# Kernel tuning notes

Measured on AMD Instinct MI355X. Metric: run time of the kernel, lower is better.

## Reference

```python
import jax, jax.numpy as jnp
import numpy as np

N = 50000          # nodes
E = 500000         # edges
NT = 10000         # target nodes
ET = 100000        # target edges
NS = 128           # node scalar dim (128x0e)
NV = 64            # node vector mult (64x1e); node dim = 128 + 64*3 = 320
ES = 64            # edge scalar dim (64x0e)
EV = 32            # edge vector mult (32x1e); edge dim = 64 + 32*3 = 160
H = 128            # hidden_dim
NA = 32            # num_atom_types
NB = 8             # num_bond_types


def setup_inputs() -> dict:
    key = jax.random.key(0)
    ks = jax.random.split(key, 40)
    nrm = lambda k, s: jax.random.normal(k, s, jnp.float32)
    w = lambda k, fi, fo: nrm(k, (fi, fo)) / np.float32(np.sqrt(fi))
    d = {}
    d['h_final'] = nrm(ks[0], (N, NS + 3 * NV))
    d['e_final'] = nrm(ks[1], (E, ES + 3 * EV))
    d['r_t_final'] = nrm(ks[2], (N, 3))
    d['target_node_idx'] = jax.random.randint(ks[3], (NT,), 0, N)
    d['target_edge_idx'] = jax.random.randint(ks[4], (ET,), 0, E)
    d['edge_index'] = jax.random.randint(ks[5], (2, E), 0, N)
    # node scalar projection (LinearRS on 0e channels)
    d['W_nsp'] = w(ks[6], NS, NS); d['b_nsp'] = jnp.zeros((NS,), jnp.float32)
    # atom type head
    d['W_at1'] = w(ks[7], NS, H); d['b_at1'] = jnp.zeros((H,), jnp.float32)
    d['W_at2'] = w(ks[8], H, NA); d['b_at2'] = jnp.zeros((NA,), jnp.float32)
    # left/right edge linears
    d['W_left'] = w(ks[9], NS, H); d['b_left'] = jnp.zeros((H,), jnp.float32)
    d['W_right'] = w(ks[10], NS, H); d['b_right'] = jnp.zeros((H,), jnp.float32)
    # edge_lin: Linear(ES+EV+H -> H), LayerNorm, SiLU, Linear(H -> 1)
    din = ES + EV + H
    d['W_el1'] = w(ks[11], din, H); d['b_el1'] = jnp.zeros((H,), jnp.float32)
    d['ln_g'] = jnp.ones((H,), jnp.float32); d['ln_b'] = jnp.zeros((H,), jnp.float32)
    d['W_el2'] = w(ks[12], H, 1); d['b_el2'] = jnp.zeros((1,), jnp.float32)
    # fully-connected tensor product to 0e: paths 0e*0e->0e and 1e*1e->0e
    d['w_tp0'] = nrm(ks[13], (NS, NS))
    d['w_tp1'] = nrm(ks[14], (NV, NV))
    # bond head MLP: Linear(1+edge_dim -> H), SiLU, Linear(H -> NB)
    d['W_bh1'] = w(ks[15], 1 + ES + 3 * EV, H); d['b_bh1'] = jnp.zeros((H,), jnp.float32)
    d['W_bh2'] = w(ks[16], H, NB); d['b_bh2'] = jnp.zeros((NB,), jnp.float32)
    return d


def reference(h_final, e_final, r_t_final, target_node_idx, target_edge_idx, edge_index,
              W_nsp, b_nsp, W_at1, b_at1, W_at2, b_at2, W_left, b_left, W_right, b_right,
              W_el1, b_el1, ln_g, ln_b, W_el2, b_el2, w_tp0, w_tp1, W_bh1, b_bh1, W_bh2, b_bh2):
    silu = jax.nn.silu
    node_proj = lambda x: x[:, :NS] @ W_nsp + b_nsp  # LinearRS restricted to 0e channels

    # --- atom type head (target nodes only) ---
    s_t = node_proj(h_final[target_node_idx])
    atom_type_logits = silu(s_t @ W_at1 + b_at1) @ W_at2 + b_at2  # [NT, NA]

    # --- per-edge force prediction ---
    row, col = edge_index[0], edge_index[1]
    hs = node_proj(h_final)                                   # [N, NS]
    inter = (hs[row] @ W_left + b_left) * (hs[col] @ W_right + b_right)  # [E, H]
    e_scalar = e_final[:, :ES]                                # [E, ES]
    e_high = e_final[:, ES:].reshape(-1, EV, 3)               # [E, EV, 3]
    e_high_norms = jnp.sqrt(jnp.sum(e_high * e_high, axis=-1))  # [E, EV]
    x = jnp.concatenate([e_scalar, e_high_norms, inter], axis=-1) @ W_el1 + b_el1
    mu = jnp.mean(x, axis=-1, keepdims=True)
    var = jnp.var(x, axis=-1, keepdims=True)
    x = (x - mu) / jnp.sqrt(var + 1e-5) * ln_g + ln_b         # LayerNorm
    weight_edge = silu(x) @ W_el2 + b_el2                     # [E, 1]
    rel = r_t_final[row] - r_t_final[col]                     # [E, 3]
    dist = jnp.linalg.norm(rel, axis=-1, keepdims=True) + 1e-8
    force = weight_edge * (rel / dist) / (dist + 1.0)
    delta = jax.ops.segment_sum(force, row, num_segments=h_final.shape[0])
    predicted_r0 = (r_t_final + delta)[target_node_idx]       # [NT, 3]

    # --- bond head: fully-connected TP(node, node) -> 0e, then MLP ---
    r2 = edge_index[0][target_edge_idx]
    c2 = edge_index[1][target_edge_idx]
    sx, vx = h_final[r2, :NS], h_final[r2, NS:].reshape(-1, NV, 3)
    sy, vy = h_final[c2, :NS], h_final[c2, NS:].reshape(-1, NV, 3)
    tp = (jnp.einsum('ei,ij,ej->e', sx, w_tp0, sy) / np.float32(NS)
          + jnp.einsum('eid,ij,ejd->e', vx, w_tp1, vy) / np.float32(NV * np.sqrt(3.0)))[:, None]
    bi = jnp.concatenate([tp, e_final[target_edge_idx]], axis=-1)  # [ET, 1+edge_dim]
    bond_logits = silu(bi @ W_bh1 + b_bh1) @ W_bh2 + b_bh2    # [ET, NB]

    return atom_type_logits, predicted_r0, bond_logits
```

## Files before the change

kernel.cpp:

```cpp
#include <hip/hip_runtime.h>
#include <math.h>

#define NN   50000
#define NE   500000
#define NTT  10000
#define ETT  100000
#define HF   320
#define EFW  160
#define NT3  7813
#define GRID3 1024

typedef __attribute__((ext_vector_type(8))) short short8_t;
typedef __attribute__((ext_vector_type(4))) float f32x4;

__device__ __forceinline__ float silu_f(float x) { return x / (1.f + __expf(-x)); }

__device__ __forceinline__ short f2bf(float f) {
    unsigned u = __float_as_uint(f);
    unsigned r = (u + 0x7fffu + ((u >> 16) & 1u)) >> 16;
    return (short)r;
}
__device__ __forceinline__ float bf2f(short s) {
    return __uint_as_float(((unsigned)(unsigned short)s) << 16);
}
__device__ __forceinline__ int swz256(int row, int col) {
    return row * 256 + (((col << 1) ^ ((row & 7) << 4)) >> 1);
}
__device__ __forceinline__ int swz128(int row, int col) {
    return row * 128 + (((col << 1) ^ ((row & 7) << 4)) >> 1);
}

__global__ __launch_bounds__(256) void k0_all(
    const float* __restrict__ W_nsp, const float* __restrict__ b_nsp,
    const float* __restrict__ W_left, const float* __restrict__ b_left,
    const float* __restrict__ W_right, const float* __restrict__ b_right,
    const float* __restrict__ W_at1, const float* __restrict__ b_at1,
    float* __restrict__ Wl, float* __restrict__ bl,
    float* __restrict__ Wr, float* __restrict__ br,
    float* __restrict__ Wc1, float* __restrict__ bc1)
{
    if (blockIdx.x < 64) {
        int idx = blockIdx.x * 256 + threadIdx.x;
        int i = idx >> 7, j = idx & 127;
        float al = 0.f, ar = 0.f;
        for (int k = 0; k < 128; ++k) {
            float w = W_nsp[i * 128 + k];
            al = fmaf(w, W_left[k * 128 + j], al);
            ar = fmaf(w, W_right[k * 128 + j], ar);
        }
        Wl[idx] = al; Wr[idx] = ar;
        if (i == 0) {
            float cl = 0.f, cr = 0.f;
            for (int k = 0; k < 128; ++k) {
                float bn = b_nsp[k];
                cl = fmaf(bn, W_left[k * 128 + j], cl);
                cr = fmaf(bn, W_right[k * 128 + j], cr);
            }
            bl[j] = cl + b_left[j];
            br[j] = cr + b_right[j];
        }
    } else {
        int idx = (blockIdx.x - 64) * 256 + threadIdx.x;
        int i = idx >> 7, j = idx & 127;
        float a = 0.f;
        for (int k = 0; k < 128; ++k)
            a = fmaf(W_nsp[i * 128 + k], W_at1[k * 128 + j], a);
        Wc1[idx] = a;
        if (i == 0) {
            float c = 0.f;
            for (int k = 0; k < 128; ++k)
                c = fmaf(b_nsp[k], W_at1[k * 128 + j], c);
            bc1[j] = c + b_at1[j];
        }
    }
}

#define KP1 136
__global__ __launch_bounds__(256) void k1_mfma(
    const float* __restrict__ h_final,
    const float* __restrict__ Wl, const float* __restrict__ bl,
    const float* __restrict__ Wr, const float* __restrict__ br,
    short* __restrict__ hlb, short* __restrict__ hrb)
{
    __shared__ __align__(16) short sx[64][KP1];
    const int tid = threadIdx.x;
    const int w = tid >> 6, lane = tid & 63, g = lane >> 4, ln = lane & 15;

    short8_t bfr[4][4];
    float bias[4];
    #pragma unroll
    for (int nf = 0; nf < 4; ++nf) {
        int col = w * 64 + nf * 16 + ln;
        const float* Wsrc = (col < 128) ? Wl : Wr;
        int cc = col & 127;
        bias[nf] = (col < 128) ? bl[cc] : br[cc];
        #pragma unroll
        for (int k0 = 0; k0 < 4; ++k0) {
            short8_t bb;
            #pragma unroll
            for (int j = 0; j < 8; ++j)
                bb[j] = f2bf(Wsrc[(k0 * 32 + g * 8 + j) * 128 + cc]);
            bfr[k0][nf] = bb;
        }
    }

    const int base = blockIdx.x * 64;
    {
        const int e = tid >> 2, q = tid & 3;
        const int n = base + e;
        #pragma unroll
        for (int i = 0; i < 8; ++i) {
            float4 v = make_float4(0.f, 0.f, 0.f, 0.f);
            if (n < NN) v = *(const float4*)&h_final[(size_t)n * HF + q * 32 + i * 4];
            short4 s4; s4.x = f2bf(v.x); s4.y = f2bf(v.y); s4.z = f2bf(v.z); s4.w = f2bf(v.w);
            *(short4*)&sx[e][q * 32 + i * 4] = s4;
        }
    }
    __syncthreads();
    f32x4 acc[4][4];
    #pragma unroll
    for (int mf = 0; mf < 4; ++mf)
        #pragma unroll
        for (int nf = 0; nf < 4; ++nf)
            acc[mf][nf] = (f32x4){0.f, 0.f, 0.f, 0.f};
    #pragma unroll
    for (int k0 = 0; k0 < 4; ++k0) {
        short8_t a[4];
        #pragma unroll
        for (int mf = 0; mf < 4; ++mf)
            a[mf] = *(const short8_t*)&sx[mf * 16 + ln][k0 * 32 + g * 8];
        #pragma unroll
        for (int mf = 0; mf < 4; ++mf)
            #pragma unroll
            for (int nf = 0; nf < 4; ++nf)
                acc[mf][nf] = __builtin_amdgcn_mfma_f32_16x16x32_bf16(
                    a[mf], bfr[k0][nf], acc[mf][nf], 0, 0, 0);
    }
    #pragma unroll
    for (int mf = 0; mf < 4; ++mf)
        #pragma unroll
        for (int nf = 0; nf < 4; ++nf) {
            int col = w * 64 + nf * 16 + ln;
            #pragma unroll
            for (int r = 0; r < 4; ++r) {
                int n = base + mf * 16 + g * 4 + r;
                if (n < NN) {
                    short v = f2bf(acc[mf][nf][r] + bias[nf]);
                    if (col < 128) hlb[(size_t)n * 128 + col] = v;
                    else           hrb[(size_t)n * 128 + col - 128] = v;
                }
            }
        }
}

__global__ __launch_bounds__(256) void k2_mfma(
    const float* __restrict__ h_final, const int* __restrict__ tn,
    const float* __restrict__ Wc1, const float* __restrict__ bc1,
    const float* __restrict__ W_at2, const float* __restrict__ b_at2,
    float* __restrict__ out)
{
    __shared__ __align__(16) short sxf[64 * 128];
    __shared__ __align__(16) short syf[64 * 128];
    const int tid = threadIdx.x;
    const int w = tid >> 6, lane = tid & 63, g = lane >> 4, ln = lane & 15;

    short8_t bfr1[4][2];
    float biasc[2];
    #pragma unroll
    for (int nf = 0; nf < 2; ++nf) {
        int col = w * 32 + nf * 16 + ln;
        biasc[nf] = bc1[col];
        #pragma unroll
        for (int k0 = 0; k0 < 4; ++k0) {
            short8_t bb;
            #pragma unroll
            for (int j = 0; j < 8; ++j)
                bb[j] = f2bf(Wc1[(k0 * 32 + g * 8 + j) * 128 + col]);
            bfr1[k0][nf] = bb;
        }
    }
    short8_t bfr2[4][2];
    float ba2v[2];
    #pragma unroll
    for (int nf = 0; nf < 2; ++nf) {
        ba2v[nf] = b_at2[nf * 16 + ln];
        #pragma unroll
        for (int k0 = 0; k0 < 4; ++k0) {
            short8_t bb;
            #pragma unroll
            for (int j = 0; j < 8; ++j)
                bb[j] = f2bf(W_at2[(k0 * 32 + g * 8 + j) * 32 + nf * 16 + ln]);
            bfr2[k0][nf] = bb;
        }
    }

    const int base = blockIdx.x * 64;
    {
        const int e = tid >> 2, q = tid & 3;
        const int t = base + e;
        const bool valid = (t < NTT);
        const int node = valid ? tn[t] : 0;
        #pragma unroll
        for (int i = 0; i < 8; ++i) {
            float4 v = make_float4(0.f, 0.f, 0.f, 0.f);
            if (valid) v = *(const float4*)&h_final[(size_t)node * HF + q * 32 + i * 4];
            short4 s4; s4.x = f2bf(v.x); s4.y = f2bf(v.y); s4.z = f2bf(v.z); s4.w = f2bf(v.w);
            *(short4*)&sxf[swz128(e, q * 32 + i * 4)] = s4;
        }
    }
    __syncthreads();
    f32x4 acc[4][2];
    #pragma unroll
    for (int mf = 0; mf < 4; ++mf)
        #pragma unroll
        for (int nf = 0; nf < 2; ++nf)
            acc[mf][nf] = (f32x4){0.f, 0.f, 0.f, 0.f};
    #pragma unroll
    for (int k0 = 0; k0 < 4; ++k0) {
        short8_t a[4];
        #pragma unroll
        for (int mf = 0; mf < 4; ++mf)
            a[mf] = *(const short8_t*)&sxf[swz128(mf * 16 + ln, k0 * 32 + g * 8)];
        #pragma unroll
        for (int mf = 0; mf < 4; ++mf)
            #pragma unroll
            for (int nf = 0; nf < 2; ++nf)
                acc[mf][nf] = __builtin_amdgcn_mfma_f32_16x16x32_bf16(
                    a[mf], bfr1[k0][nf], acc[mf][nf], 0, 0, 0);
    }
    #pragma unroll
    for (int mf = 0; mf < 4; ++mf)
        #pragma unroll
        for (int nf = 0; nf < 2; ++nf)
            #pragma unroll
            for (int r = 0; r < 4; ++r)
                syf[swz128(mf * 16 + g * 4 + r, w * 32 + nf * 16 + ln)] =
                    f2bf(silu_f(acc[mf][nf][r] + biasc[nf]));
    __syncthreads();
    f32x4 z[2];
    z[0] = (f32x4){0.f,0.f,0.f,0.f}; z[1] = (f32x4){0.f,0.f,0.f,0.f};
    #pragma unroll
    for (int k0 = 0; k0 < 4; ++k0) {
        short8_t a2 = *(const short8_t*)&syf[swz128(w * 16 + ln, k0 * 32 + g * 8)];
        #pragma unroll
        for (int nf = 0; nf < 2; ++nf)
            z[nf] = __builtin_amdgcn_mfma_f32_16x16x32_bf16(a2, bfr2[k0][nf], z[nf], 0, 0, 0);
    }
    #pragma unroll
    for (int nf = 0; nf < 2; ++nf)
        #pragma unroll
        for (int r = 0; r < 4; ++r) {
            int t = base + w * 16 + g * 4 + r;
            if (t < NTT) out[(size_t)t * 32 + nf * 16 + ln] = z[nf][r] + ba2v[nf];
        }
}

__global__ __launch_bounds__(256) void k3pre(
    const float* __restrict__ e_final, short* __restrict__ Xn)
{
    const int tid = threadIdx.x;
    const int e = blockIdx.x * 32 + (tid >> 3);
    const int sub = tid & 7;
    const float* p = &e_final[(size_t)e * EFW + 64 + sub * 12];
    float4 a = *(const float4*)p;
    float4 b = *(const float4*)(p + 4);
    float4 c = *(const float4*)(p + 8);
    short4 o;
    o.x = f2bf(sqrtf(a.x*a.x + a.y*a.y + a.z*a.z));
    o.y = f2bf(sqrtf(a.w*a.w + b.x*b.x + b.y*b.y));
    o.z = f2bf(sqrtf(b.z*b.z + b.w*b.w + c.x*c.x));
    o.w = f2bf(sqrtf(c.y*c.y + c.z*c.z + c.w*c.w));
    *(short4*)&Xn[(size_t)e * 32 + sub * 4] = o;
}

__global__ __launch_bounds__(512, 4) void k3_edge(
    const float* __restrict__ e_final, const int* __restrict__ edge_index,
    const short* __restrict__ Xn,
    const short* __restrict__ hlb, const short* __restrict__ hrb,
    const float* __restrict__ r_t,
    const float* __restrict__ W_el1, const float* __restrict__ b_el1,
    const float* __restrict__ ln_g, const float* __restrict__ ln_b,
    const float* __restrict__ W_el2, const float* __restrict__ b_el2,
    float* __restrict__ delta)
{
    __shared__ __align__(16) char smem[64 * 256 * 2];
    short* sxf = (short*)smem;
    float* syf = (float*)smem;
    __shared__ float slng[128], slnb[128], sw2[128];
    __shared__ float srel[64][4];
    __shared__ int   sidx[64];

    const int tid  = threadIdx.x;
    const int w    = tid >> 6;
    const int lane = tid & 63;
    const int g    = lane >> 4;
    const int ln   = lane & 15;
    const int es   = tid >> 3, qs = tid & 7;

    if (tid < 128) { slng[tid] = ln_g[tid]; slnb[tid] = ln_b[tid]; sw2[tid] = W_el2[tid]; }

    short8_t bfr[7];
    #pragma unroll
    for (int k0 = 0; k0 < 7; ++k0) {
        short8_t bb;
        #pragma unroll
        for (int j = 0; j < 8; ++j)
            bb[j] = f2bf(W_el1[(k0 * 32 + g * 8 + j) * 128 + w * 16 + ln]);
        bfr[k0] = bb;
    }
    const float bias0 = b_el1[w * 16 + ln];
    const float b2 = b_el2[0];

    for (int t = blockIdx.x; t < NT3; t += GRID3) {
        __syncthreads();

        {
            const int ge = t * 64 + es;
            const bool valid = (ge < NE);
            int r = 0, c = 0;
            if (valid) { r = edge_index[ge]; c = edge_index[NE + ge]; }
            #pragma unroll
            for (int i = 0; i < 2; ++i) {
                float4 v = make_float4(0.f, 0.f, 0.f, 0.f);
                if (valid) v = *(const float4*)&e_final[(size_t)ge * EFW + qs * 8 + i * 4];
                short4 s4; s4.x = f2bf(v.x); s4.y = f2bf(v.y);
                s4.z = f2bf(v.z); s4.w = f2bf(v.w);
                *(short4*)&sxf[swz256(es, qs * 8 + i * 4)] = s4;
            }
            {
                short4 n0 = make_short4(0,0,0,0);
                if (valid) n0 = *(const short4*)&Xn[(size_t)ge * 32 + qs * 4];
                *(short4*)&sxf[swz256(es, 64 + qs * 4)] = n0;
            }
            #pragma unroll
            for (int i = 0; i < 2; ++i) {
                short8_t hv, rv, pr;
                if (valid) {
                    hv = *(const short8_t*)&hlb[(size_t)r * 128 + qs * 16 + i * 8];
                    rv = *(const short8_t*)&hrb[(size_t)c * 128 + qs * 16 + i * 8];
                } else {
                    #pragma unroll
                    for (int jj = 0; jj < 8; ++jj) { hv[jj] = 0; rv[jj] = 0; }
                }
                #pragma unroll
                for (int jj = 0; jj < 8; ++jj)
                    pr[jj] = f2bf(bf2f(hv[jj]) * bf2f(rv[jj]));
                *(short8_t*)&sxf[swz256(es, 96 + qs * 16 + i * 8)] = pr;
            }
            if (qs == 0) {
                float rx = 0.f, ry = 0.f, rz = 0.f;
                if (valid) {
                    rx = r_t[r*3+0] - r_t[c*3+0];
                    ry = r_t[r*3+1] - r_t[c*3+1];
                    rz = r_t[r*3+2] - r_t[c*3+2];
                }
                sidx[es] = r;
                srel[es][0] = rx; srel[es][1] = ry; srel[es][2] = rz;
            }
        }
        __syncthreads();

        f32x4 acc[4];
        #pragma unroll
        for (int mf = 0; mf < 4; ++mf)
            acc[mf] = (f32x4){0.f, 0.f, 0.f, 0.f};
        #pragma unroll
        for (int k0 = 0; k0 < 7; ++k0) {
            short8_t a[4];
            #pragma unroll
            for (int mf = 0; mf < 4; ++mf)
                a[mf] = *(const short8_t*)&sxf[swz256(mf * 16 + ln, k0 * 32 + g * 8)];
            #pragma unroll
            for (int mf = 0; mf < 4; ++mf)
                acc[mf] = __builtin_amdgcn_mfma_f32_16x16x32_bf16(
                    a[mf], bfr[k0], acc[mf], 0, 0, 0);
        }
        __syncthreads();

        #pragma unroll
        for (int mf = 0; mf < 4; ++mf)
            #pragma unroll
            for (int r = 0; r < 4; ++r) {
                int row = mf * 16 + g * 4 + r;
                int col = (w * 16 + ln) ^ ((row & 7) << 2);
                syf[row * 128 + col] = acc[mf][r] + bias0;
            }
        __syncthreads();

        {
            float yv[16];
            float s = 0.f, q = 0.f;
            #pragma unroll
            for (int i = 0; i < 4; ++i) {
                int col4 = (qs * 16 + i * 4) ^ ((es & 7) << 2);
                float4 v = *(const float4*)&syf[es * 128 + col4];
                yv[i*4+0] = v.x; yv[i*4+1] = v.y; yv[i*4+2] = v.z; yv[i*4+3] = v.w;
                s += v.x + v.y + v.z + v.w;
                q += v.x*v.x + v.y*v.y + v.z*v.z + v.w*v.w;
            }
            s += __shfl_xor(s, 1); q += __shfl_xor(q, 1);
            s += __shfl_xor(s, 2); q += __shfl_xor(q, 2);
            s += __shfl_xor(s, 4); q += __shfl_xor(q, 4);
            const float mu = s * (1.f / 128.f);
            const float iv = rsqrtf(q * (1.f / 128.f) - mu * mu + 1e-5f);
            float p = 0.f;
            #pragma unroll
            for (int i = 0; i < 4; ++i) {
                int c0 = qs * 16 + i * 4;
                float4 gv = *(const float4*)&slng[c0];
                float4 bv = *(const float4*)&slnb[c0];
                float4 wv = *(const float4*)&sw2[c0];
                p += silu_f((yv[i*4+0] - mu) * iv * gv.x + bv.x) * wv.x;
                p += silu_f((yv[i*4+1] - mu) * iv * gv.y + bv.y) * wv.y;
                p += silu_f((yv[i*4+2] - mu) * iv * gv.z + bv.z) * wv.z;
                p += silu_f((yv[i*4+3] - mu) * iv * gv.w + bv.w) * wv.w;
            }
            p += __shfl_xor(p, 1); p += __shfl_xor(p, 2); p += __shfl_xor(p, 4);
            if (qs == 0) {
                int ge = t * 64 + es;
                if (ge < NE) {
                    float we = p + b2;
                    float rx = srel[es][0], ry = srel[es][1], rz = srel[es][2];
                    float d = sqrtf(rx*rx + ry*ry + rz*rz) + 1e-8f;
                    float f = we / (d * (d + 1.f));
                    int rr = sidx[es];
                    atomicAdd(&delta[rr*3+0], f*rx);
                    atomicAdd(&delta[rr*3+1], f*ry);
                    atomicAdd(&delta[rr*3+2], f*rz);
                }
            }
        }
    }
}

__global__ __launch_bounds__(256) void k4a_g(
    const float* __restrict__ h_final, const float* __restrict__ w_tp0,
    short* __restrict__ Gb)
{
    __shared__ __align__(16) short sx[64][KP1];
    const int tid = threadIdx.x;
    const int w = tid >> 6, lane = tid & 63, g = lane >> 4, ln = lane & 15;

    short8_t bfr[4][2];
    #pragma unroll
    for (int k0 = 0; k0 < 4; ++k0)
        #pragma unroll
        for (int nf = 0; nf < 2; ++nf) {
            short8_t bb;
            #pragma unroll
            for (int j = 0; j < 8; ++j)
                bb[j] = f2bf(w_tp0[(k0 * 32 + g * 8 + j) * 128 + w * 32 + nf * 16 + ln]);
            bfr[k0][nf] = bb;
        }

    const int base = blockIdx.x * 64;
    {
        const int e = tid >> 2, q = tid & 3;
        const int n = base + e;
        #pragma unroll
        for (int i = 0; i < 8; ++i) {
            float4 v = make_float4(0.f, 0.f, 0.f, 0.f);
            if (n < NN) v = *(const float4*)&h_final[(size_t)n * HF + q * 32 + i * 4];
            short4 s4; s4.x = f2bf(v.x); s4.y = f2bf(v.y); s4.z = f2bf(v.z); s4.w = f2bf(v.w);
            *(short4*)&sx[e][q * 32 + i * 4] = s4;
        }
    }
    __syncthreads();
    f32x4 acc[4][2];
    #pragma unroll
    for (int mf = 0; mf < 4; ++mf)
        #pragma unroll
        for (int nf = 0; nf < 2; ++nf)
            acc[mf][nf] = (f32x4){0.f, 0.f, 0.f, 0.f};
    #pragma unroll
    for (int k0 = 0; k0 < 4; ++k0) {
        short8_t a[4];
        #pragma unroll
        for (int mf = 0; mf < 4; ++mf)
            a[mf] = *(const short8_t*)&sx[mf * 16 + ln][k0 * 32 + g * 8];
        #pragma unroll
        for (int mf = 0; mf < 4; ++mf)
            #pragma unroll
            for (int nf = 0; nf < 2; ++nf)
                acc[mf][nf] = __builtin_amdgcn_mfma_f32_16x16x32_bf16(
                    a[mf], bfr[k0][nf], acc[mf][nf], 0, 0, 0);
    }
    #pragma unroll
    for (int mf = 0; mf < 4; ++mf)
        #pragma unroll
        for (int nf = 0; nf < 2; ++nf) {
            int col = w * 32 + nf * 16 + ln;
            #pragma unroll
            for (int r = 0; r < 4; ++r) {
                int n = base + mf * 16 + g * 4 + r;
                if (n < NN) Gb[(size_t)n * 128 + col] = f2bf(acc[mf][nf][r]);
            }
        }
}

__global__ __launch_bounds__(256) void k4b_gv(
    const float* __restrict__ h_final, const float* __restrict__ w_tp1,
    short* __restrict__ Gvb)
{
    __shared__ float sW1T[64 * 65];
    __shared__ float sv[4][192];
    const int tid = threadIdx.x, w = tid >> 6, lane = tid & 63;
    for (int idx = tid; idx < 4096; idx += 256) {
        int i = idx >> 6, j = idx & 63;
        sW1T[j * 65 + i] = w_tp1[idx];
    }
    for (int base = blockIdx.x * 4; base < NN; base += gridDim.x * 4) {
        __syncthreads();
        if (tid < 192) {
            int nd = tid / 48, c4 = tid % 48;
            int n = base + nd;
            float4 v = make_float4(0.f, 0.f, 0.f, 0.f);
            if (n < NN) v = *(const float4*)&h_final[(size_t)n * HF + 128 + c4 * 4];
            *(float4*)&sv[nd][c4 * 4] = v;
        }
        __syncthreads();
        int n = base + w;
        if (n < NN) {
            float a0 = 0.f, a1 = 0.f, a2 = 0.f;
            for (int j = 0; j < 64; ++j) {
                float wv = sW1T[j * 65 + lane];
                a0 = fmaf(wv, sv[w][3 * j],     a0);
                a1 = fmaf(wv, sv[w][3 * j + 1], a1);
                a2 = fmaf(wv, sv[w][3 * j + 2], a2);
            }
            short* gp = &Gvb[(size_t)n * 192 + lane * 3];
            gp[0] = f2bf(a0); gp[1] = f2bf(a1); gp[2] = f2bf(a2);
        }
    }
}

#define KP5 200
__global__ __launch_bounds__(256) void k5_mfma(
    const float* __restrict__ e_final, const int* __restrict__ te,
    const float* __restrict__ h_final, const int* __restrict__ edge_index,
    const short* __restrict__ Gb, const short* __restrict__ Gvb,
    const float* __restrict__ W_bh1, const float* __restrict__ b_bh1,
    const float* __restrict__ W_bh2, const float* __restrict__ b_bh2,
    float* __restrict__ out)
{
    __shared__ __align__(16) short sx[64][KP5];
    __shared__ __align__(16) short sy[64][136];
    __shared__ float stp[64];
    const int tid = threadIdx.x, w = tid >> 6, lane = tid & 63, g = lane >> 4, ln = lane & 15;
    const int base = blockIdx.x * 64;

    {
        const int e = tid >> 2, q = tid & 3;
        const int ge = base + e;
        const bool valid = (ge < ETT);
        const int gid = valid ? te[ge] : 0;
        const int r2 = edge_index[gid], c2 = edge_index[NE + gid];
        float s1 = 0.f, s2 = 0.f;
        #pragma unroll
        for (int i = 0; i < 4; ++i) {
            short8_t gv = *(const short8_t*)&Gb[(size_t)r2 * 128 + q * 32 + i * 8];
            float4 h0 = *(const float4*)&h_final[(size_t)c2 * HF + q * 32 + i * 8];
            float4 h1 = *(const float4*)&h_final[(size_t)c2 * HF + q * 32 + i * 8 + 4];
            s1 += bf2f(gv[0])*h0.x + bf2f(gv[1])*h0.y + bf2f(gv[2])*h0.z + bf2f(gv[3])*h0.w
                + bf2f(gv[4])*h1.x + bf2f(gv[5])*h1.y + bf2f(gv[6])*h1.z + bf2f(gv[7])*h1.w;
        }
        #pragma unroll
        for (int i = 0; i < 6; ++i) {
            short8_t gv = *(const short8_t*)&Gvb[(size_t)c2 * 192 + q * 48 + i * 8];
            float4 h0 = *(const float4*)&h_final[(size_t)r2 * HF + 128 + q * 48 + i * 8];
            float4 h1 = *(const float4*)&h_final[(size_t)r2 * HF + 128 + q * 48 + i * 8 + 4];
            s2 += bf2f(gv[0])*h0.x + bf2f(gv[1])*h0.y + bf2f(gv[2])*h0.z + bf2f(gv[3])*h0.w
                + bf2f(gv[4])*h1.x + bf2f(gv[5])*h1.y + bf2f(gv[6])*h1.z + bf2f(gv[7])*h1.w;
        }
        float res = s1 * (1.f / 128.f) + s2 * (1.f / 110.85125168440814f);
        res += __shfl_xor(res, 1); res += __shfl_xor(res, 2);
        if (q == 0) stp[e] = res;
    }

    short8_t bfr[6][2];
    #pragma unroll
    for (int k0 = 0; k0 < 6; ++k0)
        #pragma unroll
        for (int nf = 0; nf < 2; ++nf) {
            short8_t bb;
            #pragma unroll
            for (int j = 0; j < 8; ++j) {
                int k = k0 * 32 + g * 8 + j;
                float v = 0.f;
                if (k < 160)       v = W_bh1[(size_t)(k + 1) * 128 + w * 32 + nf * 16 + ln];
                else if (k == 160) v = W_bh1[w * 32 + nf * 16 + ln];
                bb[j] = f2bf(v);
            }
            bfr[k0][nf] = bb;
        }
    const float bias0 = b_bh1[w * 32 + ln];
    const float bias1 = b_bh1[w * 32 + 16 + ln];

    short8_t bfr2[4];
    #pragma unroll
    for (int k0 = 0; k0 < 4; ++k0) {
        short8_t bb;
        #pragma unroll
        for (int j = 0; j < 8; ++j) {
            int k = k0 * 32 + g * 8 + j;
            bb[j] = (ln < 8) ? f2bf(W_bh2[k * 8 + ln]) : (short)0;
        }
        bfr2[k0] = bb;
    }
    const float b2o = (ln < 8) ? b_bh2[ln] : 0.f;

    for (int idx = tid; idx < 64 * 39; idx += 256) {
        int rr = idx / 39, c = 161 + idx % 39;
        sx[rr][c] = 0;
    }
    {
        const int e = tid >> 2, q = tid & 3;
        const int ge = base + e;
        const bool valid = (ge < ETT);
        const int gid = valid ? te[ge] : 0;
        #pragma unroll
        for (int i = 0; i < 10; ++i) {
            float4 v = make_float4(0.f, 0.f, 0.f, 0.f);
            if (valid) v = *(const float4*)&e_final[(size_t)gid * EFW + q * 40 + i * 4];
            short4 s4; s4.x = f2bf(v.x); s4.y = f2bf(v.y); s4.z = f2bf(v.z); s4.w = f2bf(v.w);
            *(short4*)&sx[e][q * 40 + i * 4] = s4;
        }
    }
    __syncthreads();
    if (tid < 64) sx[tid][160] = f2bf(stp[tid]);
    __syncthreads();

    f32x4 acc[4][2];
    #pragma unroll
    for (int mf = 0; mf < 4; ++mf)
        #pragma unroll
        for (int nf = 0; nf < 2; ++nf)
            acc[mf][nf] = (f32x4){0.f, 0.f, 0.f, 0.f};
    #pragma unroll
    for (int k0 = 0; k0 < 6; ++k0) {
        short8_t a[4];
        #pragma unroll
        for (int mf = 0; mf < 4; ++mf)
            a[mf] = *(const short8_t*)&sx[mf * 16 + ln][k0 * 32 + g * 8];
        #pragma unroll
        for (int mf = 0; mf < 4; ++mf)
            #pragma unroll
            for (int nf = 0; nf < 2; ++nf)
                acc[mf][nf] = __builtin_amdgcn_mfma_f32_16x16x32_bf16(
                    a[mf], bfr[k0][nf], acc[mf][nf], 0, 0, 0);
    }
    #pragma unroll
    for (int mf = 0; mf < 4; ++mf)
        #pragma unroll
        for (int nf = 0; nf < 2; ++nf)
            #pragma unroll
            for (int r = 0; r < 4; ++r)
                sy[mf * 16 + g * 4 + r][w * 32 + nf * 16 + ln] =
                    f2bf(silu_f(acc[mf][nf][r] + (nf ? bias1 : bias0)));
    __syncthreads();

    f32x4 z = (f32x4){0.f, 0.f, 0.f, 0.f};
    #pragma unroll
    for (int k0 = 0; k0 < 4; ++k0) {
        short8_t a2 = *(const short8_t*)&sy[w * 16 + ln][k0 * 32 + g * 8];
        z = __builtin_amdgcn_mfma_f32_16x16x32_bf16(a2, bfr2[k0], z, 0, 0, 0);
    }
    #pragma unroll
    for (int r = 0; r < 4; ++r) {
        int e = base + w * 16 + g * 4 + r;
        if (ln < 8 && e < ETT) out[(size_t)e * 8 + ln] = z[r] + b2o;
    }
}

__global__ void k6_r0(const float* __restrict__ r_t, const float* __restrict__ delta,
                      const int* __restrict__ tn, float* __restrict__ out)
{
    int i = blockIdx.x * 256 + threadIdx.x;
    if (i < NTT * 3) {
        int t = i / 3, d = i - t * 3;
        int n = tn[t];
        out[i] = r_t[n * 3 + d] + delta[n * 3 + d];
    }
}

extern "C" void kernel_launch(void* const* d_in, const int* in_sizes, int n_in,
                              void* d_out, int out_size, void* d_ws, size_t ws_size,
                              hipStream_t stream)
{
    const float* h_final = (const float*)d_in[0];
    const float* e_final = (const float*)d_in[1];
    const float* r_t     = (const float*)d_in[2];
    const int*   tn      = (const int*)d_in[3];
    const int*   te      = (const int*)d_in[4];
    const int*   ei      = (const int*)d_in[5];
    const float* W_nsp   = (const float*)d_in[6];
    const float* b_nsp   = (const float*)d_in[7];
    const float* W_at1   = (const float*)d_in[8];
    const float* b_at1   = (const float*)d_in[9];
    const float* W_at2   = (const float*)d_in[10];
    const float* b_at2   = (const float*)d_in[11];
    const float* W_left  = (const float*)d_in[12];
    const float* b_left  = (const float*)d_in[13];
    const float* W_right = (const float*)d_in[14];
    const float* b_right = (const float*)d_in[15];
    const float* W_el1   = (const float*)d_in[16];
    const float* b_el1   = (const float*)d_in[17];
    const float* ln_g    = (const float*)d_in[18];
    const float* ln_b    = (const float*)d_in[19];
    const float* W_el2   = (const float*)d_in[20];
    const float* b_el2   = (const float*)d_in[21];
    const float* w_tp0   = (const float*)d_in[22];
    const float* w_tp1   = (const float*)d_in[23];
    const float* W_bh1   = (const float*)d_in[24];
    const float* b_bh1   = (const float*)d_in[25];
    const float* W_bh2   = (const float*)d_in[26];
    const float* b_bh2   = (const float*)d_in[27];

    float* ws    = (float*)d_ws;
    float* Wl    = ws;
    float* bl    = Wl + 16384;
    float* Wr    = bl + 128;
    float* br    = Wr + 16384;
    float* Wc1   = ws + 33024;
    float* bc1   = Wc1 + 16384;
    short* hlb   = (short*)(ws + 49536);
    short* hrb   = hlb + 6400000;
    short* Xn    = hrb + 6400000;
    float* delta = (float*)(Xn + 16000000);
    float* tpb   = delta + 150000;
    short* Gvb   = (short*)(tpb + 100000);
    short* Gb    = hlb;

    float* out      = (float*)d_out;
    float* out_atom = out;
    float* out_r0   = out + 320000;
    float* out_bond = out + 350000;

    k0_all<<<128, 256, 0, stream>>>(W_nsp, b_nsp, W_left, b_left, W_right, b_right,
                                    W_at1, b_at1, Wl, bl, Wr, br, Wc1, bc1);
    k3pre<<<15625, 256, 0, stream>>>(e_final, Xn);
    k1_mfma<<<782, 256, 0, stream>>>(h_final, Wl, bl, Wr, br, hlb, hrb);
    k2_mfma<<<157, 256, 0, stream>>>(h_final, tn, Wc1, bc1, W_at2, b_at2, out_atom);
    hipMemsetAsync(delta, 0, 150000 * sizeof(float), stream);
    k3_edge<<<GRID3, 512, 0, stream>>>(e_final, ei, Xn, hlb, hrb, r_t, W_el1, b_el1,
                                       ln_g, ln_b, W_el2, b_el2, delta);
    k6_r0<<<(NTT * 3 + 255) / 256, 256, 0, stream>>>(r_t, delta, tn, out_r0);
    k4a_g<<<782, 256, 0, stream>>>(h_final, w_tp0, Gb);
    k4b_gv<<<2048, 256, 0, stream>>>(h_final, w_tp1, Gvb);
    k5_mfma<<<1563, 256, 0, stream>>>(e_final, te, h_final, ei, Gb, Gvb,
                                      W_bh1, b_bh1, W_bh2, b_bh2, out_bond);
}
```

Baseline: 416.4 us.

## Merge independent kernels into fewer launches via block-index dispatch

Independent kernels are combined into fused launches that branch on block index. Weight precompute, edge-norm preprocessing and delta zeroing form one launch. The left/right projection, atom head and Gv tensor-product precompute form a second, and the Gb precompute plus the r0 gather form a third. This cuts the launch count from nine (plus a memset) to five and lets independent work from different stages share the GPU. The price is heavier per-launch register and shared-memory footprints, which can lower occupancy for the lighter branches. The Gv precompute also moves ahead of the edge kernel.

```diff
diff --git a/kernel.cpp b/kernel.cpp
--- a/kernel.cpp
+++ b/kernel.cpp
@@ -30,247 +30,279 @@
     return row * 128 + (((col << 1) ^ ((row & 7) << 4)) >> 1);
 }
 
-__global__ __launch_bounds__(256) void k0_all(
+#define KP1 136
+__global__ __launch_bounds__(256) void ka_pre(
+    const float* __restrict__ e_final, short* __restrict__ Xn,
     const float* __restrict__ W_nsp, const float* __restrict__ b_nsp,
     const float* __restrict__ W_left, const float* __restrict__ b_left,
     const float* __restrict__ W_right, const float* __restrict__ b_right,
     const float* __restrict__ W_at1, const float* __restrict__ b_at1,
     float* __restrict__ Wl, float* __restrict__ bl,
     float* __restrict__ Wr, float* __restrict__ br,
-    float* __restrict__ Wc1, float* __restrict__ bc1)
+    float* __restrict__ Wc1, float* __restrict__ bc1,
+    float* __restrict__ delta)
 {
-    if (blockIdx.x < 64) {
-        int idx = blockIdx.x * 256 + threadIdx.x;
-        int i = idx >> 7, j = idx & 127;
-        float al = 0.f, ar = 0.f;
-        for (int k = 0; k < 128; ++k) {
-            float w = W_nsp[i * 128 + k];
-            al = fmaf(w, W_left[k * 128 + j], al);
-            ar = fmaf(w, W_right[k * 128 + j], ar);
-        }
-        Wl[idx] = al; Wr[idx] = ar;
-        if (i == 0) {
-            float cl = 0.f, cr = 0.f;
+    const int tid = threadIdx.x;
+    const int vb = blockIdx.x;
+    if (vb < 15625) {
+        const int e = vb * 32 + (tid >> 3);
+        const int sub = tid & 7;
+        const float* p = &e_final[(size_t)e * EFW + 64 + sub * 12];
+        float4 a = *(const float4*)p;
+        float4 b = *(const float4*)(p + 4);
+        float4 c = *(const float4*)(p + 8);
+        short4 o;
+        o.x = f2bf(sqrtf(a.x*a.x + a.y*a.y + a.z*a.z));
+        o.y = f2bf(sqrtf(a.w*a.w + b.x*b.x + b.y*b.y));
+        o.z = f2bf(sqrtf(b.z*b.z + b.w*b.w + c.x*c.x));
+        o.w = f2bf(sqrtf(c.y*c.y + c.z*c.z + c.w*c.w));
+        *(short4*)&Xn[(size_t)e * 32 + sub * 4] = o;
+    } else if (vb < 15753) {
+        const int b0 = vb - 15625;
+        if (b0 < 64) {
+            int idx = b0 * 256 + tid;
+            int i = idx >> 7, j = idx & 127;
+            float al = 0.f, ar = 0.f;
             for (int k = 0; k < 128; ++k) {
-                float bn = b_nsp[k];
-                cl = fmaf(bn, W_left[k * 128 + j], cl);
-                cr = fmaf(bn, W_right[k * 128 + j], cr);
-            }
-            bl[j] = cl + b_left[j];
-            br[j] = cr + b_right[j];
+                float w = W_nsp[i * 128 + k];
+                al = fmaf(w, W_left[k * 128 + j], al);
+                ar = fmaf(w, W_right[k * 128 + j], ar);
+            }
+            Wl[idx] = al; Wr[idx] = ar;
+            if (i == 0) {
+                float cl = 0.f, cr = 0.f;
+                for (int k = 0; k < 128; ++k) {
+                    float bn = b_nsp[k];
+                    cl = fmaf(bn, W_left[k * 128 + j], cl);
+                    cr = fmaf(bn, W_right[k * 128 + j], cr);
+                }
+                bl[j] = cl + b_left[j];
+                br[j] = cr + b_right[j];
+            }
+        } else {
+            int idx = (b0 - 64) * 256 + tid;
+            int i = idx >> 7, j = idx & 127;
+            float a = 0.f;
+            for (int k = 0; k < 128; ++k)
+                a = fmaf(W_nsp[i * 128 + k], W_at1[k * 128 + j], a);
+            Wc1[idx] = a;
+            if (i == 0) {
+                float c = 0.f;
+                for (int k = 0; k < 128; ++k)
+                    c = fmaf(b_nsp[k], W_at1[k * 128 + j], c);
+                bc1[j] = c + b_at1[j];
+            }
         }
     } else {
-        int idx = (blockIdx.x - 64) * 256 + threadIdx.x;
-        int i = idx >> 7, j = idx & 127;
-        float a = 0.f;
-        for (int k = 0; k < 128; ++k)
-            a = fmaf(W_nsp[i * 128 + k], W_at1[k * 128 + j], a);
-        Wc1[idx] = a;
-        if (i == 0) {
-            float c = 0.f;
-            for (int k = 0; k < 128; ++k)
-                c = fmaf(b_nsp[k], W_at1[k * 128 + j], c);
-            bc1[j] = c + b_at1[j];
-        }
-    }
-}
-
-#define KP1 136
-__global__ __launch_bounds__(256) void k1_mfma(
-    const float* __restrict__ h_final,
+        int i = (vb - 15753) * 256 + tid;
+        if (i < 150000) delta[i] = 0.f;
+    }
+}
+
+__global__ __launch_bounds__(256) void kb_mid(
+    const float* __restrict__ h_final, const int* __restrict__ tn,
     const float* __restrict__ Wl, const float* __restrict__ bl,
     const float* __restrict__ Wr, const float* __restrict__ br,
-    short* __restrict__ hlb, short* __restrict__ hrb)
+    const float* __restrict__ Wc1, const float* __restrict__ bc1,
+    const float* __restrict__ W_at2, const float* __restrict__ b_at2,
+    const float* __restrict__ w_tp1,
+    short* __restrict__ hlb, short* __restrict__ hrb,
+    short* __restrict__ Gvb, float* __restrict__ out_atom)
 {
-    __shared__ __align__(16) short sx[64][KP1];
+    __shared__ __align__(16) char smemB[32768];
     const int tid = threadIdx.x;
-    const int w = tid >> 6, lane = tid & 63, g = lane >> 4, ln = lane & 15;
-
-    short8_t bfr[4][4];
-    float bias[4];
-    #pragma unroll
-    for (int nf = 0; nf < 4; ++nf) {
-        int col = w * 64 + nf * 16 + ln;
-        const float* Wsrc = (col < 128) ? Wl : Wr;
-        int cc = col & 127;
-        bias[nf] = (col < 128) ? bl[cc] : br[cc];
-        #pragma unroll
-        for (int k0 = 0; k0 < 4; ++k0) {
-            short8_t bb;
-            #pragma unroll
-            for (int j = 0; j < 8; ++j)
-                bb[j] = f2bf(Wsrc[(k0 * 32 + g * 8 + j) * 128 + cc]);
-            bfr[k0][nf] = bb;
-        }
-    }
-
-    const int base = blockIdx.x * 64;
-    {
-        const int e = tid >> 2, q = tid & 3;
-        const int n = base + e;
-        #pragma unroll
-        for (int i = 0; i < 8; ++i) {
-            float4 v = make_float4(0.f, 0.f, 0.f, 0.f);
-            if (n < NN) v = *(const float4*)&h_final[(size_t)n * HF + q * 32 + i * 4];
-            short4 s4; s4.x = f2bf(v.x); s4.y = f2bf(v.y); s4.z = f2bf(v.z); s4.w = f2bf(v.w);
-            *(short4*)&sx[e][q * 32 + i * 4] = s4;
-        }
-    }
-    __syncthreads();
-    f32x4 acc[4][4];
-    #pragma unroll
-    for (int mf = 0; mf < 4; ++mf)
-        #pragma unroll
-        for (int nf = 0; nf < 4; ++nf)
-            acc[mf][nf] = (f32x4){0.f, 0.f, 0.f, 0.f};
-    #pragma unroll
-    for (int k0 = 0; k0 < 4; ++k0) {
-        short8_t a[4];
-        #pragma unroll
-        for (int mf = 0; mf < 4; ++mf)
-            a[mf] = *(const short8_t*)&sx[mf * 16 + ln][k0 * 32 + g * 8];
-        #pragma unroll
-        for (int mf = 0; mf < 4; ++mf)
-            #pragma unroll
-            for (int nf = 0; nf < 4; ++nf)
-                acc[mf][nf] = __builtin_amdgcn_mfma_f32_16x16x32_bf16(
-                    a[mf], bfr[k0][nf], acc[mf][nf], 0, 0, 0);
-    }
-    #pragma unroll
-    for (int mf = 0; mf < 4; ++mf)
+    const int vb = blockIdx.x;
+    if (vb < 2048) {
+        float* sW1T = (float*)smemB;
+        float (*sv)[192] = (float(*)[192])(smemB + 16640);
+        const int w = tid >> 6, lane = tid & 63;
+        for (int idx = tid; idx < 4096; idx += 256) {
+            int i = idx >> 6, j = idx & 63;
+            sW1T[j * 65 + i] = w_tp1[idx];
+        }
+        for (int base = vb * 4; base < NN; base += 2048 * 4) {
+            __syncthreads();
+            if (tid < 192) {
+                int nd = tid / 48, c4 = tid % 48;
+                int n = base + nd;
+                float4 v = make_float4(0.f, 0.f, 0.f, 0.f);
+                if (n < NN) v = *(const float4*)&h_final[(size_t)n * HF + 128 + c4 * 4];
+                *(float4*)&sv[nd][c4 * 4] = v;
+            }
+            __syncthreads();
+            int n = base + w;
+            if (n < NN) {
+                float a0 = 0.f, a1 = 0.f, a2 = 0.f;
+                for (int j = 0; j < 64; ++j) {
+                    float wv = sW1T[j * 65 + lane];
+                    a0 = fmaf(wv, sv[w][3 * j],     a0);
+                    a1 = fmaf(wv, sv[w][3 * j + 1], a1);
+                    a2 = fmaf(wv, sv[w][3 * j + 2], a2);
+                }
+                short* gp = &Gvb[(size_t)n * 192 + lane * 3];
+                gp[0] = f2bf(a0); gp[1] = f2bf(a1); gp[2] = f2bf(a2);
+            }
+        }
+    } else if (vb < 2830) {
+        short (*sx)[KP1] = (short(*)[KP1])smemB;
+        const int w = tid >> 6, lane = tid & 63, g = lane >> 4, ln = lane & 15;
+        short8_t bfr[4][4];
+        float bias[4];
         #pragma unroll
         for (int nf = 0; nf < 4; ++nf) {
             int col = w * 64 + nf * 16 + ln;
+            const float* Wsrc = (col < 128) ? Wl : Wr;
+            int cc = col & 127;
+            bias[nf] = (col < 128) ? bl[cc] : br[cc];
+            #pragma unroll
+            for (int k0 = 0; k0 < 4; ++k0) {
+                short8_t bb;
+                #pragma unroll
+                for (int j = 0; j < 8; ++j)
+                    bb[j] = f2bf(Wsrc[(k0 * 32 + g * 8 + j) * 128 + cc]);
+                bfr[k0][nf] = bb;
+            }
+        }
+        const int base = (vb - 2048) * 64;
+        {
+            const int e = tid >> 2, q = tid & 3;
+            const int n = base + e;
+            #pragma unroll
+            for (int i = 0; i < 8; ++i) {
+                float4 v = make_float4(0.f, 0.f, 0.f, 0.f);
+                if (n < NN) v = *(const float4*)&h_final[(size_t)n * HF + q * 32 + i * 4];
+                short4 s4; s4.x = f2bf(v.x); s4.y = f2bf(v.y); s4.z = f2bf(v.z); s4.w = f2bf(v.w);
+                *(short4*)&sx[e][q * 32 + i * 4] = s4;
+            }
+        }
+        __syncthreads();
+        f32x4 acc[4][4];
+        #pragma unroll
+        for (int mf = 0; mf < 4; ++mf)
+            #pragma unroll
+            for (int nf = 0; nf < 4; ++nf)
+                acc[mf][nf] = (f32x4){0.f, 0.f, 0.f, 0.f};
+        #pragma unroll
+        for (int k0 = 0; k0 < 4; ++k0) {
+            short8_t a[4];
+            #pragma unroll
+            for (int mf = 0; mf < 4; ++mf)
+                a[mf] = *(const short8_t*)&sx[mf * 16 + ln][k0 * 32 + g * 8];
+            #pragma unroll
+            for (int mf = 0; mf < 4; ++mf)
+                #pragma unroll
+                for (int nf = 0; nf < 4; ++nf)
+                    acc[mf][nf] = __builtin_amdgcn_mfma_f32_16x16x32_bf16(
+                        a[mf], bfr[k0][nf], acc[mf][nf], 0, 0, 0);
+        }
+        #pragma unroll
+        for (int mf = 0; mf < 4; ++mf)
+            #pragma unroll
+            for (int nf = 0; nf < 4; ++nf) {
+                int col = w * 64 + nf * 16 + ln;
+                #pragma unroll
+                for (int r = 0; r < 4; ++r) {
+                    int n = base + mf * 16 + g * 4 + r;
+                    if (n < NN) {
+                        short v = f2bf(acc[mf][nf][r] + bias[nf]);
+                        if (col < 128) hlb[(size_t)n * 128 + col] = v;
+                        else           hrb[(size_t)n * 128 + col - 128] = v;
+                    }
+                }
+            }
+    } else {
+        short* sxf = (short*)smemB;
+        short* syf = (short*)(smemB + 16384);
+        const int w = tid >> 6, lane = tid & 63, g = lane >> 4, ln = lane & 15;
+        short8_t bfr1[4][2];
+        float biasc[2];
+        #pragma unroll
+        for (int nf = 0; nf < 2; ++nf) {
+            int col = w * 32 + nf * 16 + ln;
+            biasc[nf] = bc1[col];
+            #pragma unroll
+            for (int k0 = 0; k0 < 4; ++k0) {
+                short8_t bb;
+                #pragma unroll
+                for (int j = 0; j < 8; ++j)
+                    bb[j] = f2bf(Wc1[(k0 * 32 + g * 8 + j) * 128 + col]);
+                bfr1[k0][nf] = bb;
+            }
+        }
+        short8_t bfr2[4][2];
+        float ba2v[2];
+        #pragma unroll
+        for (int nf = 0; nf < 2; ++nf) {
+            ba2v[nf] = b_at2[nf * 16 + ln];
+            #pragma unroll
+            for (int k0 = 0; k0 < 4; ++k0) {
+                short8_t bb;
+                #pragma unroll
+                for (int j = 0; j < 8; ++j)
+                    bb[j] = f2bf(W_at2[(k0 * 32 + g * 8 + j) * 32 + nf * 16 + ln]);
+                bfr2[k0][nf] = bb;
+            }
+        }
+        const int base = (vb - 2830) * 64;
+        {
+            const int e = tid >> 2, q = tid & 3;
+            const int t = base + e;
+            const bool valid = (t < NTT);
+            const int node = valid ? tn[t] : 0;
+            #pragma unroll
+            for (int i = 0; i < 8; ++i) {
+                float4 v = make_float4(0.f, 0.f, 0.f, 0.f);
+                if (valid) v = *(const float4*)&h_final[(size_t)node * HF + q * 32 + i * 4];
+                short4 s4; s4.x = f2bf(v.x); s4.y = f2bf(v.y); s4.z = f2bf(v.z); s4.w = f2bf(v.w);
+                *(short4*)&sxf[swz128(e, q * 32 + i * 4)] = s4;
+            }
+        }
+        __syncthreads();
+        f32x4 acc[4][2];
+        #pragma unroll
+        for (int mf = 0; mf < 4; ++mf)
+            #pragma unroll
+            for (int nf = 0; nf < 2; ++nf)
+                acc[mf][nf] = (f32x4){0.f, 0.f, 0.f, 0.f};
+        #pragma unroll
+        for (int k0 = 0; k0 < 4; ++k0) {
+            short8_t a[4];
+            #pragma unroll
+            for (int mf = 0; mf < 4; ++mf)
+                a[mf] = *(const short8_t*)&sxf[swz128(mf * 16 + ln, k0 * 32 + g * 8)];
+            #pragma unroll
+            for (int mf = 0; mf < 4; ++mf)
+                #pragma unroll
+                for (int nf = 0; nf < 2; ++nf)
+                    acc[mf][nf] = __builtin_amdgcn_mfma_f32_16x16x32_bf16(
+                        a[mf], bfr1[k0][nf], acc[mf][nf], 0, 0, 0);
+        }
+        #pragma unroll
+        for (int mf = 0; mf < 4; ++mf)
+            #pragma unroll
+            for (int nf = 0; nf < 2; ++nf)
+                #pragma unroll
+                for (int r = 0; r < 4; ++r)
+                    syf[swz128(mf * 16 + g * 4 + r, w * 32 + nf * 16 + ln)] =
+                        f2bf(silu_f(acc[mf][nf][r] + biasc[nf]));
+        __syncthreads();
+        f32x4 z[2];
+        z[0] = (f32x4){0.f,0.f,0.f,0.f}; z[1] = (f32x4){0.f,0.f,0.f,0.f};
+        #pragma unroll
+        for (int k0 = 0; k0 < 4; ++k0) {
+            short8_t a2 = *(const short8_t*)&syf[swz128(w * 16 + ln, k0 * 32 + g * 8)];
+            #pragma unroll
+            for (int nf = 0; nf < 2; ++nf)
+                z[nf] = __builtin_amdgcn_mfma_f32_16x16x32_bf16(a2, bfr2[k0][nf], z[nf], 0, 0, 0);
+        }
+        #pragma unroll
+        for (int nf = 0; nf < 2; ++nf)
             #pragma unroll
             for (int r = 0; r < 4; ++r) {
-                int n = base + mf * 16 + g * 4 + r;
-                if (n < NN) {
-                    short v = f2bf(acc[mf][nf][r] + bias[nf]);
-                    if (col < 128) hlb[(size_t)n * 128 + col] = v;
-                    else           hrb[(size_t)n * 128 + col - 128] = v;
-                }
-            }
-        }
-}
-
-__global__ __launch_bounds__(256) void k2_mfma(
-    const float* __restrict__ h_final, const int* __restrict__ tn,
-    const float* __restrict__ Wc1, const float* __restrict__ bc1,
-    const float* __restrict__ W_at2, const float* __restrict__ b_at2,
-    float* __restrict__ out)
-{
-    __shared__ __align__(16) short sxf[64 * 128];
-    __shared__ __align__(16) short syf[64 * 128];
-    const int tid = threadIdx.x;
-    const int w = tid >> 6, lane = tid & 63, g = lane >> 4, ln = lane & 15;
-
-    short8_t bfr1[4][2];
-    float biasc[2];
-    #pragma unroll
-    for (int nf = 0; nf < 2; ++nf) {
-        int col = w * 32 + nf * 16 + ln;
-        biasc[nf] = bc1[col];
-        #pragma unroll
-        for (int k0 = 0; k0 < 4; ++k0) {
-            short8_t bb;
-            #pragma unroll
-            for (int j = 0; j < 8; ++j)
-                bb[j] = f2bf(Wc1[(k0 * 32 + g * 8 + j) * 128 + col]);
-            bfr1[k0][nf] = bb;
-        }
-    }
-    short8_t bfr2[4][2];
-    float ba2v[2];
-    #pragma unroll
-    for (int nf = 0; nf < 2; ++nf) {
-        ba2v[nf] = b_at2[nf * 16 + ln];
-        #pragma unroll
-        for (int k0 = 0; k0 < 4; ++k0) {
-            short8_t bb;
-            #pragma unroll
-            for (int j = 0; j < 8; ++j)
-                bb[j] = f2bf(W_at2[(k0 * 32 + g * 8 + j) * 32 + nf * 16 + ln]);
-            bfr2[k0][nf] = bb;
-        }
-    }
-
-    const int base = blockIdx.x * 64;
-    {
-        const int e = tid >> 2, q = tid & 3;
-        const int t = base + e;
-        const bool valid = (t < NTT);
-        const int node = valid ? tn[t] : 0;
-        #pragma unroll
-        for (int i = 0; i < 8; ++i) {
-            float4 v = make_float4(0.f, 0.f, 0.f, 0.f);
-            if (valid) v = *(const float4*)&h_final[(size_t)node * HF + q * 32 + i * 4];
-            short4 s4; s4.x = f2bf(v.x); s4.y = f2bf(v.y); s4.z = f2bf(v.z); s4.w = f2bf(v.w);
-            *(short4*)&sxf[swz128(e, q * 32 + i * 4)] = s4;
-        }
-    }
-    __syncthreads();
-    f32x4 acc[4][2];
-    #pragma unroll
-    for (int mf = 0; mf < 4; ++mf)
-        #pragma unroll
-        for (int nf = 0; nf < 2; ++nf)
-            acc[mf][nf] = (f32x4){0.f, 0.f, 0.f, 0.f};
-    #pragma unroll
-    for (int k0 = 0; k0 < 4; ++k0) {
-        short8_t a[4];
-        #pragma unroll
-        for (int mf = 0; mf < 4; ++mf)
-            a[mf] = *(const short8_t*)&sxf[swz128(mf * 16 + ln, k0 * 32 + g * 8)];
-        #pragma unroll
-        for (int mf = 0; mf < 4; ++mf)
-            #pragma unroll
-            for (int nf = 0; nf < 2; ++nf)
-                acc[mf][nf] = __builtin_amdgcn_mfma_f32_16x16x32_bf16(
-                    a[mf], bfr1[k0][nf], acc[mf][nf], 0, 0, 0);
-    }
-    #pragma unroll
-    for (int mf = 0; mf < 4; ++mf)
-        #pragma unroll
-        for (int nf = 0; nf < 2; ++nf)
-            #pragma unroll
-            for (int r = 0; r < 4; ++r)
-                syf[swz128(mf * 16 + g * 4 + r, w * 32 + nf * 16 + ln)] =
-                    f2bf(silu_f(acc[mf][nf][r] + biasc[nf]));
-    __syncthreads();
-    f32x4 z[2];
-    z[0] = (f32x4){0.f,0.f,0.f,0.f}; z[1] = (f32x4){0.f,0.f,0.f,0.f};
-    #pragma unroll
-    for (int k0 = 0; k0 < 4; ++k0) {
-        short8_t a2 = *(const short8_t*)&syf[swz128(w * 16 + ln, k0 * 32 + g * 8)];
-        #pragma unroll
-        for (int nf = 0; nf < 2; ++nf)
-            z[nf] = __builtin_amdgcn_mfma_f32_16x16x32_bf16(a2, bfr2[k0][nf], z[nf], 0, 0, 0);
-    }
-    #pragma unroll
-    for (int nf = 0; nf < 2; ++nf)
-        #pragma unroll
-        for (int r = 0; r < 4; ++r) {
-            int t = base + w * 16 + g * 4 + r;
-            if (t < NTT) out[(size_t)t * 32 + nf * 16 + ln] = z[nf][r] + ba2v[nf];
-        }
-}
-
-__global__ __launch_bounds__(256) void k3pre(
-    const float* __restrict__ e_final, short* __restrict__ Xn)
-{
-    const int tid = threadIdx.x;
-    const int e = blockIdx.x * 32 + (tid >> 3);
-    const int sub = tid & 7;
-    const float* p = &e_final[(size_t)e * EFW + 64 + sub * 12];
-    float4 a = *(const float4*)p;
-    float4 b = *(const float4*)(p + 4);
-    float4 c = *(const float4*)(p + 8);
-    short4 o;
-    o.x = f2bf(sqrtf(a.x*a.x + a.y*a.y + a.z*a.z));
-    o.y = f2bf(sqrtf(a.w*a.w + b.x*b.x + b.y*b.y));
-    o.z = f2bf(sqrtf(b.z*b.z + b.w*b.w + c.x*c.x));
-    o.w = f2bf(sqrtf(c.y*c.y + c.z*c.z + c.w*c.w));
-    *(short4*)&Xn[(size_t)e * 32 + sub * 4] = o;
+                int t = base + w * 16 + g * 4 + r;
+                if (t < NTT) out_atom[(size_t)t * 32 + nf * 16 + ln] = z[nf][r] + ba2v[nf];
+            }
+    }
 }
 
 __global__ __launch_bounds__(512, 4) void k3_edge(
@@ -433,103 +465,78 @@
     }
 }
 
-__global__ __launch_bounds__(256) void k4a_g(
+__global__ __launch_bounds__(256) void kd_post(
     const float* __restrict__ h_final, const float* __restrict__ w_tp0,
-    short* __restrict__ Gb)
+    short* __restrict__ Gb,
+    const float* __restrict__ r_t, const float* __restrict__ delta,
+    const int* __restrict__ tn, float* __restrict__ out_r0)
 {
-    __shared__ __align__(16) short sx[64][KP1];
+    __shared__ __align__(16) char smemD[64 * KP1 * 2];
     const int tid = threadIdx.x;
-    const int w = tid >> 6, lane = tid & 63, g = lane >> 4, ln = lane & 15;
-
-    short8_t bfr[4][2];
-    #pragma unroll
-    for (int k0 = 0; k0 < 4; ++k0)
-        #pragma unroll
-        for (int nf = 0; nf < 2; ++nf) {
-            short8_t bb;
-            #pragma unroll
-            for (int j = 0; j < 8; ++j)
-                bb[j] = f2bf(w_tp0[(k0 * 32 + g * 8 + j) * 128 + w * 32 + nf * 16 + ln]);
-            bfr[k0][nf] = bb;
-        }
-
-    const int base = blockIdx.x * 64;
-    {
-        const int e = tid >> 2, q = tid & 3;
-        const int n = base + e;
-        #pragma unroll
-        for (int i = 0; i < 8; ++i) {
-            float4 v = make_float4(0.f, 0.f, 0.f, 0.f);
-            if (n < NN) v = *(const float4*)&h_final[(size_t)n * HF + q * 32 + i * 4];
-            short4 s4; s4.x = f2bf(v.x); s4.y = f2bf(v.y); s4.z = f2bf(v.z); s4.w = f2bf(v.w);
-            *(short4*)&sx[e][q * 32 + i * 4] = s4;
-        }
-    }
-    __syncthreads();
-    f32x4 acc[4][2];
-    #pragma unroll
-    for (int mf = 0; mf < 4; ++mf)
-        #pragma unroll
-        for (int nf = 0; nf < 2; ++nf)
-            acc[mf][nf] = (f32x4){0.f, 0.f, 0.f, 0.f};
-    #pragma unroll
-    for (int k0 = 0; k0 < 4; ++k0) {
-        short8_t a[4];
-        #pragma unroll
-        for (int mf = 0; mf < 4; ++mf)
-            a[mf] = *(const short8_t*)&sx[mf * 16 + ln][k0 * 32 + g * 8];
+    const int vb = blockIdx.x;
+    if (vb < 782) {
+        short (*sx)[KP1] = (short(*)[KP1])smemD;
+        const int w = tid >> 6, lane = tid & 63, g = lane >> 4, ln = lane & 15;
+        short8_t bfr[4][2];
+        #pragma unroll
+        for (int k0 = 0; k0 < 4; ++k0)
+            #pragma unroll
+            for (int nf = 0; nf < 2; ++nf) {
+                short8_t bb;
+                #pragma unroll
+                for (int j = 0; j < 8; ++j)
+                    bb[j] = f2bf(w_tp0[(k0 * 32 + g * 8 + j) * 128 + w * 32 + nf * 16 + ln]);
+                bfr[k0][nf] = bb;
+            }
+        const int base = vb * 64;
+        {
+            const int e = tid >> 2, q = tid & 3;
+            const int n = base + e;
+            #pragma unroll
+            for (int i = 0; i < 8; ++i) {
+                float4 v = make_float4(0.f, 0.f, 0.f, 0.f);
+                if (n < NN) v = *(const float4*)&h_final[(size_t)n * HF + q * 32 + i * 4];
+                short4 s4; s4.x = f2bf(v.x); s4.y = f2bf(v.y); s4.z = f2bf(v.z); s4.w = f2bf(v.w);
+                *(short4*)&sx[e][q * 32 + i * 4] = s4;
+            }
+        }
+        __syncthreads();
+        f32x4 acc[4][2];
         #pragma unroll
         for (int mf = 0; mf < 4; ++mf)
             #pragma unroll
             for (int nf = 0; nf < 2; ++nf)
-                acc[mf][nf] = __builtin_amdgcn_mfma_f32_16x16x32_bf16(
-                    a[mf], bfr[k0][nf], acc[mf][nf], 0, 0, 0);
-    }
-    #pragma unroll
-    for (int mf = 0; mf < 4; ++mf)
-        #pragma unroll
-        for (int nf = 0; nf < 2; ++nf) {
-            int col = w * 32 + nf * 16 + ln;
-            #pragma unroll
-            for (int r = 0; r < 4; ++r) {
-                int n = base + mf * 16 + g * 4 + r;
-                if (n < NN) Gb[(size_t)n * 128 + col] = f2bf(acc[mf][nf][r]);
-            }
-        }
-}
-
-__global__ __launch_bounds__(256) void k4b_gv(
-    const float* __restrict__ h_final, const float* __restrict__ w_tp1,
-    short* __restrict__ Gvb)
-{
-    __shared__ float sW1T[64 * 65];
-    __shared__ float sv[4][192];
-    const int tid = threadIdx.x, w = tid >> 6, lane = tid & 63;
-    for (int idx = tid; idx < 4096; idx += 256) {
-        int i = idx >> 6, j = idx & 63;
-        sW1T[j * 65 + i] = w_tp1[idx];
-    }
-    for (int base = blockIdx.x * 4; base < NN; base += gridDim.x * 4) {
-        __syncthreads();
-        if (tid < 192) {
-            int nd = tid / 48, c4 = tid % 48;
-            int n = base + nd;
-            float4 v = make_float4(0.f, 0.f, 0.f, 0.f);
-            if (n < NN) v = *(const float4*)&h_final[(size_t)n * HF + 128 + c4 * 4];
-            *(float4*)&sv[nd][c4 * 4] = v;
-        }
-        __syncthreads();
-        int n = base + w;
-        if (n < NN) {
-            float a0 = 0.f, a1 = 0.f, a2 = 0.f;
-            for (int j = 0; j < 64; ++j) {
-                float wv = sW1T[j * 65 + lane];
-                a0 = fmaf(wv, sv[w][3 * j],     a0);
-                a1 = fmaf(wv, sv[w][3 * j + 1], a1);
-                a2 = fmaf(wv, sv[w][3 * j + 2], a2);
-            }
-            short* gp = &Gvb[(size_t)n * 192 + lane * 3];
-            gp[0] = f2bf(a0); gp[1] = f2bf(a1); gp[2] = f2bf(a2);
+                acc[mf][nf] = (f32x4){0.f, 0.f, 0.f, 0.f};
+        #pragma unroll
+        for (int k0 = 0; k0 < 4; ++k0) {
+            short8_t a[4];
+            #pragma unroll
+            for (int mf = 0; mf < 4; ++mf)
+                a[mf] = *(const short8_t*)&sx[mf * 16 + ln][k0 * 32 + g * 8];
+            #pragma unroll
+            for (int mf = 0; mf < 4; ++mf)
+                #pragma unroll
+                for (int nf = 0; nf < 2; ++nf)
+                    acc[mf][nf] = __builtin_amdgcn_mfma_f32_16x16x32_bf16(
+                        a[mf], bfr[k0][nf], acc[mf][nf], 0, 0, 0);
+        }
+        #pragma unroll
+        for (int mf = 0; mf < 4; ++mf)
+            #pragma unroll
+            for (int nf = 0; nf < 2; ++nf) {
+                int col = w * 32 + nf * 16 + ln;
+                #pragma unroll
+                for (int r = 0; r < 4; ++r) {
+                    int n = base + mf * 16 + g * 4 + r;
+                    if (n < NN) Gb[(size_t)n * 128 + col] = f2bf(acc[mf][nf][r]);
+                }
+            }
+    } else {
+        int i = (vb - 782) * 256 + tid;
+        if (i < NTT * 3) {
+            int t = i / 3, d = i - t * 3;
+            int n = tn[t];
+            out_r0[i] = r_t[n * 3 + d] + delta[n * 3 + d];
         }
     }
 }
@@ -669,17 +676,6 @@
     for (int r = 0; r < 4; ++r) {
         int e = base + w * 16 + g * 4 + r;
         if (ln < 8 && e < ETT) out[(size_t)e * 8 + ln] = z[r] + b2o;
-    }
-}
-
-__global__ void k6_r0(const float* __restrict__ r_t, const float* __restrict__ delta,
-                      const int* __restrict__ tn, float* __restrict__ out)
-{
-    int i = blockIdx.x * 256 + threadIdx.x;
-    if (i < NTT * 3) {
-        int t = i / 3, d = i - t * 3;
-        int n = tn[t];
-        out[i] = r_t[n * 3 + d] + delta[n * 3 + d];
     }
 }
 
@@ -736,17 +732,14 @@
     float* out_r0   = out + 320000;
     float* out_bond = out + 350000;
 
-    k0_all<<<128, 256, 0, stream>>>(W_nsp, b_nsp, W_left, b_left, W_right, b_right,
-                                    W_at1, b_at1, Wl, bl, Wr, br, Wc1, bc1);
-    k3pre<<<15625, 256, 0, stream>>>(e_final, Xn);
-    k1_mfma<<<782, 256, 0, stream>>>(h_final, Wl, bl, Wr, br, hlb, hrb);
-    k2_mfma<<<157, 256, 0, stream>>>(h_final, tn, Wc1, bc1, W_at2, b_at2, out_atom);
-    hipMemsetAsync(delta, 0, 150000 * sizeof(float), stream);
+    ka_pre<<<16340, 256, 0, stream>>>(e_final, Xn, W_nsp, b_nsp, W_left, b_left,
+                                      W_right, b_right, W_at1, b_at1,
+                                      Wl, bl, Wr, br, Wc1, bc1, delta);
+    kb_mid<<<2987, 256, 0, stream>>>(h_final, tn, Wl, bl, Wr, br, Wc1, bc1,
+                                     W_at2, b_at2, w_tp1, hlb, hrb, Gvb, out_atom);
     k3_edge<<<GRID3, 512, 0, stream>>>(e_final, ei, Xn, hlb, hrb, r_t, W_el1, b_el1,
                                        ln_g, ln_b, W_el2, b_el2, delta);
-    k6_r0<<<(NTT * 3 + 255) / 256, 256, 0, stream>>>(r_t, delta, tn, out_r0);
-    k4a_g<<<782, 256, 0, stream>>>(h_final, w_tp0, Gb);
-    k4b_gv<<<2048, 256, 0, stream>>>(h_final, w_tp1, Gvb);
+    kd_post<<<900, 256, 0, stream>>>(h_final, w_tp0, Gb, r_t, delta, tn, out_r0);
     k5_mfma<<<1563, 256, 0, stream>>>(e_final, te, h_final, ei, Gb, Gvb,
                                       W_bh1, b_bh1, W_bh2, b_bh2, out_bond);
 }
```

Result: slower. 444.4 us (+6.7%).
